# Performance work log

Hardware: AMD Instinct MI355X
Metric: run time of the kernel (lower is better)

Reference implementation:

```python
import jax, jax.numpy as jnp
import numpy as np

N_NODES = 100000

def gcn_conv(x, W, b, src, dst, norm, n):
    # PyG GCNConv: h = x @ W, then normalized sum-aggregation at target nodes, + bias
    h = x @ W                                   # [N, out]
    msg = h[src] * norm[:, None]                # gather + scale, [E, out]
    out = jax.ops.segment_sum(msg, dst, num_segments=n)
    return out + b

def build_norm(src, dst, n):
    # symmetric normalization with unit edge weights (gcn_norm)
    deg = jax.ops.segment_sum(jnp.ones(src.shape[0], jnp.float32), dst, num_segments=n)
    dinv = jnp.where(deg > 0, jax.lax.rsqrt(jnp.maximum(deg, 1.0)), 0.0)
    return dinv[src] * dinv[dst]

def setup_inputs() -> dict:
    key = jax.random.key(0)
    ks = jax.random.split(key, 10)
    n, e, din, dout = N_NODES, 1600000, 256, 86
    x = jax.random.normal(ks[0], (n, din), jnp.float32)
    edge_index = jax.random.randint(ks[1], (2, e), 0, n, jnp.int64)
    def glorot(k, i, o):
        s = jnp.sqrt(6.0 / (i + o))
        return jax.random.uniform(k, (i, o), jnp.float32, -s, s)
    return {
        'x': x, 'edge_index': edge_index,
        'W1': glorot(ks[2], din, 128), 'b1': jnp.zeros((128,), jnp.float32),
        'W2': glorot(ks[3], 128, 64),  'b2': jnp.zeros((64,), jnp.float32),
        'W3': glorot(ks[4], 64, 32),   'b3': jnp.zeros((32,), jnp.float32),
        'Wc': glorot(ks[5], 32, dout), 'bc': jnp.zeros((dout,), jnp.float32),
    }

def reference(x, edge_index, W1, b1, W2, b2, W3, b3, Wc, bc):
    n = x.shape[0]
    # add self-loops (GCNConv default add_self_loops=True)
    loops = jnp.arange(n, dtype=edge_index.dtype)
    src = jnp.concatenate([edge_index[0], loops])
    dst = jnp.concatenate([edge_index[1], loops])
    norm = build_norm(src, dst, n)
    h = jnp.tanh(gcn_conv(x, W1, b1, src, dst, norm, n))
    h = jnp.tanh(gcn_conv(h, W2, b2, src, dst, norm, n))
    h = jnp.tanh(gcn_conv(h, W3, b3, src, dst, norm, n))
    out = h @ Wc + bc
    return (out, h)
```

## Files before the change

### kernel.cpp

```cpp
#include <hip/hip_runtime.h>
#include <hip/hip_bf16.h>


__global__ void count_kernel(const int* __restrict__ dst, int* __restrict__ count, int E) {
    int e = blockIdx.x * blockDim.x + threadIdx.x;
    if (e < E) atomicAdd(&count[dst[e]], 1);
}

__global__ void scan1_kernel(const int* __restrict__ count, int* __restrict__ incl,
                             float* __restrict__ dinv, int* __restrict__ blocksum, int n) {
    __shared__ int lds[1024];
    int t = threadIdx.x;
    int i = blockIdx.x * 1024 + t;
    int v = (i < n) ? count[i] : 0;
    if (i < n) dinv[i] = rsqrtf((float)(v + 1));
    lds[t] = v;
    __syncthreads();
    for (int off = 1; off < 1024; off <<= 1) {
        int add = (t >= off) ? lds[t - off] : 0;
        __syncthreads();
        lds[t] += add;
        __syncthreads();
    }
    if (i < n) incl[i] = lds[t];
    if (t == 1023) blocksum[blockIdx.x] = lds[1023];
}

__global__ void scan2_kernel(const int* __restrict__ blocksum, int* __restrict__ blockoff,
                             int* __restrict__ rowptr, int nb, int n, int E) {
    __shared__ int lds[1024];
    int t = threadIdx.x;
    int v = (t < nb) ? blocksum[t] : 0;
    lds[t] = v;
    __syncthreads();
    for (int off = 1; off < 1024; off <<= 1) {
        int add = (t >= off) ? lds[t - off] : 0;
        __syncthreads();
        lds[t] += add;
        __syncthreads();
    }
    if (t < nb) blockoff[t] = lds[t] - v;
    if (t == 0) rowptr[n] = E;
}

__global__ void scan3_kernel(int* __restrict__ rowptr, const int* __restrict__ count,
                             const int* __restrict__ blockoff, int n) {
    int i = blockIdx.x * blockDim.x + threadIdx.x;
    if (i < n) rowptr[i] = rowptr[i] - count[i] + blockoff[i >> 10];
}

__global__ void scatter_kernel(const int* __restrict__ src, const int* __restrict__ dst,
                               const int* __restrict__ rowptr, int* __restrict__ cursor,
                               int* __restrict__ esrc, int E) {
    int e = blockIdx.x * blockDim.x + threadIdx.x;
    if (e < E) {
        int d = dst[e];
        int pos = rowptr[d] + atomicAdd(&cursor[d], 1);
        esrc[pos] = src[e];
    }
}

template<int DIN, int DOUT, int TN>
__global__ __launch_bounds__(256) void matmul_scale_kernel(
        const float* __restrict__ X, const float* __restrict__ W,
        const float* __restrict__ dinv, float* __restrict__ G, int n) {
    constexpr int TM = 8;
    constexpr int NCG = DOUT / TN;
    constexpr int NRG = 256 / NCG;
    constexpr int BM = NRG * TM;
    constexpr int BK = 32;
    constexpr int XS = BM + 4;

    __shared__ float Xt[BK][XS];
    __shared__ float Ws[BK][DOUT];

    int tid = threadIdx.x;
    int tx = tid % NCG;
    int ty = tid / NCG;
    int row0 = blockIdx.x * BM;

    float acc[TM][TN];
    #pragma unroll
    for (int r = 0; r < TM; r++)
        #pragma unroll
        for (int c = 0; c < TN; c++) acc[r][c] = 0.f;

    for (int k0 = 0; k0 < DIN; k0 += BK) {
        #pragma unroll
        for (int i = tid; i < BM * (BK / 4); i += 256) {
            int r  = i >> 3;
            int c4 = (i & 7) << 2;
            int rg = row0 + r;
            float4 v = make_float4(0.f, 0.f, 0.f, 0.f);
            if (rg < n) v = *(const float4*)&X[(size_t)rg * DIN + k0 + c4];
            const float* vp = (const float*)&v;
            #pragma unroll
            for (int j = 0; j < 4; j++) {
                int c  = c4 + j;
                int rs = r ^ (((c >> 2) & 3) << 3);
                Xt[c][rs] = vp[j];
            }
        }
        #pragma unroll
        for (int i = tid; i < BK * (DOUT / 4); i += 256) {
            int r  = i / (DOUT / 4);
            int c4 = (i % (DOUT / 4)) << 2;
            *(float4*)&Ws[r][c4] = *(const float4*)&W[(size_t)(k0 + r) * DOUT + c4];
        }
        __syncthreads();

        #pragma unroll 4
        for (int k = 0; k < BK; k++) {
            int mask = ((k >> 2) & 3) << 3;
            int rr = (ty * TM) ^ mask;
            float xv[TM];
            *(float4*)&xv[0] = *(const float4*)&Xt[k][rr];
            *(float4*)&xv[4] = *(const float4*)&Xt[k][rr + 4];
            float wv[TN];
            #pragma unroll
            for (int c4 = 0; c4 < TN; c4 += 4)
                *(float4*)&wv[c4] = *(const float4*)&Ws[k][tx * TN + c4];
            #pragma unroll
            for (int r = 0; r < TM; r++)
                #pragma unroll
                for (int c = 0; c < TN; c++)
                    acc[r][c] += xv[r] * wv[c];
        }
        __syncthreads();
    }

    #pragma unroll
    for (int r = 0; r < TM; r++) {
        int rg = row0 + ty * TM + r;
        if (rg < n) {
            float di = dinv[rg];
            float ov[TN];
            #pragma unroll
            for (int c = 0; c < TN; c++) ov[c] = acc[r][c] * di;
            #pragma unroll
            for (int c4 = 0; c4 < TN; c4 += 4)
                *(float4*)&G[(size_t)rg * DOUT + tx * TN + c4] = *(float4*)&ov[c4];
        }
    }
}

template<int DOUT>
__global__ void agg_kernel(const float* __restrict__ g, const float* __restrict__ dinv,
                           const int* __restrict__ rowptr, const int* __restrict__ esrc,
                           const float* __restrict__ bias, float* __restrict__ out, int n) {
    constexpr int LPN = DOUT / 2;
    constexpr int NPW = 64 / LPN;
    int wave = threadIdx.x >> 6;
    int lane = threadIdx.x & 63;
    int sub  = lane / LPN;
    int cl   = lane % LPN;
    int node = (blockIdx.x * (blockDim.x >> 6) + wave) * NPW + sub;
    if (node >= n) return;

    const float2* g2 = (const float2*)g;
    float2 acc = g2[(size_t)node * LPN + cl];

    int e = rowptr[node], end = rowptr[node + 1];
    for (; e + 4 <= end; e += 4) {
        int s0 = esrc[e], s1 = esrc[e + 1], s2 = esrc[e + 2], s3 = esrc[e + 3];
        float2 v0 = g2[(size_t)s0 * LPN + cl];
        float2 v1 = g2[(size_t)s1 * LPN + cl];
        float2 v2 = g2[(size_t)s2 * LPN + cl];
        float2 v3 = g2[(size_t)s3 * LPN + cl];
        acc.x += v0.x + v1.x + v2.x + v3.x;
        acc.y += v0.y + v1.y + v2.y + v3.y;
    }
    for (; e < end; e++) {
        int s = esrc[e];
        float2 v = g2[(size_t)s * LPN + cl];
        acc.x += v.x;
        acc.y += v.y;
    }
    float di = dinv[node];
    float2 b = ((const float2*)bias)[cl];
    float2 o;
    o.x = tanhf(di * acc.x + b.x);
    o.y = tanhf(di * acc.y + b.y);
    ((float2*)out)[(size_t)node * LPN + cl] = o;
}

__global__ __launch_bounds__(256) void cls_kernel(
        const float* __restrict__ H, const float* __restrict__ Wc,
        const float* __restrict__ bc, float* __restrict__ out, int n) {
    constexpr int DIN = 32, DOUT = 86, RPB = 64;
    __shared__ float Hs[RPB][DIN + 4];
    __shared__ float Ws[DIN][DOUT];
    __shared__ float bs[DOUT];
    int tid = threadIdx.x;
    int row0 = blockIdx.x * RPB;
    for (int i = tid; i < DIN * DOUT; i += 256) Ws[i / DOUT][i % DOUT] = Wc[i];
    if (tid < DOUT) bs[tid] = bc[tid];
    for (int i = tid; i < RPB * (DIN / 4); i += 256) {
        int r = i >> 3, c4 = (i & 7) << 2;
        int rg = row0 + r;
        float4 v = make_float4(0.f, 0.f, 0.f, 0.f);
        if (rg < n) v = *(const float4*)&H[(size_t)rg * DIN + c4];
        *(float4*)&Hs[r][c4] = v;
    }
    __syncthreads();
    for (int idx = tid; idx < RPB * DOUT; idx += 256) {
        int r = idx / DOUT, c = idx - r * DOUT;
        float a = bs[c];
        #pragma unroll
        for (int k = 0; k < DIN; k++) a += Hs[r][k] * Ws[k][c];
        int rg = row0 + r;
        if (rg < n) out[(size_t)rg * DOUT + c] = a;
    }
}

extern "C" void kernel_launch(void* const* d_in, const int* in_sizes, int n_in,
                              void* d_out, int out_size, void* d_ws, size_t ws_size,
                              hipStream_t stream) {
    const float* x  = (const float*)d_in[0];
    const int*   ei = (const int*)d_in[1];
    const float* W1 = (const float*)d_in[2];
    const float* b1 = (const float*)d_in[3];
    const float* W2 = (const float*)d_in[4];
    const float* b2 = (const float*)d_in[5];
    const float* W3 = (const float*)d_in[6];
    const float* b3 = (const float*)d_in[7];
    const float* Wc = (const float*)d_in[8];
    const float* bc = (const float*)d_in[9];

    const int n = in_sizes[0] / 256;
    const int E = in_sizes[1] / 2;
    const int* src = ei;
    const int* dst = ei + E;

    char* ws = (char*)d_ws;
    size_t off = 0;
    auto alloc = [&](size_t bytes) {
        void* p = ws + off;
        off = (off + bytes + 255) & ~(size_t)255;
        return p;
    };
    float* dinv    = (float*)alloc((size_t)n * 4);
    int*   count   = (int*)  alloc((size_t)n * 4);
    int*   rowptr  = (int*)  alloc((size_t)(n + 1) * 4);
    int*   cursor  = (int*)  alloc((size_t)n * 4);
    int*   blocksum= (int*)  alloc(1024 * 4);
    int*   blockoff= (int*)  alloc(1024 * 4);
    int*   esrc    = (int*)  alloc((size_t)E * 4);
    float* bufA    = (float*)alloc((size_t)n * 128 * 4);
    float* bufB    = (float*)alloc((size_t)n * 128 * 4);

    float* outp = (float*)d_out;
    float* h3   = outp + (size_t)n * 86;

    hipMemsetAsync(count, 0, (size_t)n * 4, stream);
    hipMemsetAsync(cursor, 0, (size_t)n * 4, stream);

    int eblocks = (E + 255) / 256;
    count_kernel<<<eblocks, 256, 0, stream>>>(dst, count, E);
    int nb = (n + 1023) / 1024;
    scan1_kernel<<<nb, 1024, 0, stream>>>(count, rowptr, dinv, blocksum, n);
    scan2_kernel<<<1, 1024, 0, stream>>>(blocksum, blockoff, rowptr, nb, n, E);
    scan3_kernel<<<(n + 255) / 256, 256, 0, stream>>>(rowptr, count, blockoff, n);
    scatter_kernel<<<eblocks, 256, 0, stream>>>(src, dst, rowptr, cursor, esrc, E);

    matmul_scale_kernel<256, 128, 8><<<(n + 127) / 128, 256, 0, stream>>>(x, W1, dinv, bufA, n);
    agg_kernel<128><<<(n + 3) / 4, 256, 0, stream>>>(bufA, dinv, rowptr, esrc, b1, bufB, n);
    matmul_scale_kernel<128, 64, 4><<<(n + 127) / 128, 256, 0, stream>>>(bufB, W2, dinv, bufA, n);
    agg_kernel<64><<<(n + 7) / 8, 256, 0, stream>>>(bufA, dinv, rowptr, esrc, b2, bufB, n);
    matmul_scale_kernel<64, 32, 4><<<(n + 255) / 256, 256, 0, stream>>>(bufB, W3, dinv, bufA, n);
    agg_kernel<32><<<(n + 15) / 16, 256, 0, stream>>>(bufA, dinv, rowptr, esrc, b3, h3, n);
    cls_kernel<<<(n + 63) / 64, 256, 0, stream>>>(h3, Wc, bc, outp, n);
}
```

Before: 709.7 us.

## Store scaled GEMM outputs in fp16 to halve aggregation gather traffic

The per-layer transformed features are written as packed half precision instead of fp32. The aggregation kernels then gather 8-byte fp16 quads per lane and accumulate in fp32. The matmul kernel is retiled to 128-thread blocks with smaller row tiles and interleaved column groups, and the launch geometry changes to match. The aim is to cut the random-gather memory traffic in aggregation, which dominates, at the cost of fp16 rounding error in the intermediate features.

```diff
diff --git a/kernel.cpp b/kernel.cpp
--- a/kernel.cpp
+++ b/kernel.cpp
@@ -1,5 +1,6 @@
 #include <hip/hip_runtime.h>
 #include <hip/hip_bf16.h>
+#include <hip/hip_fp16.h>
 
 
 __global__ void count_kernel(const int* __restrict__ dst, int* __restrict__ count, int E) {
@@ -60,14 +61,14 @@
     }
 }
 
-template<int DIN, int DOUT, int TN>
-__global__ __launch_bounds__(256) void matmul_scale_kernel(
+template<int DIN, int DOUT, int QN, int BM>
+__global__ __launch_bounds__(128) void matmul_scale_kernel(
         const float* __restrict__ X, const float* __restrict__ W,
-        const float* __restrict__ dinv, float* __restrict__ G, int n) {
+        const float* __restrict__ dinv, __half* __restrict__ G, int n) {
     constexpr int TM = 8;
-    constexpr int NCG = DOUT / TN;
-    constexpr int NRG = 256 / NCG;
-    constexpr int BM = NRG * TM;
+    constexpr int NCG = DOUT / (4 * QN);
+    constexpr int NRG = BM / TM;
+    static_assert(NCG * NRG == 128, "block must be 128 threads");
     constexpr int BK = 32;
     constexpr int XS = BM + 4;
 
@@ -79,30 +80,28 @@
     int ty = tid / NCG;
     int row0 = blockIdx.x * BM;
 
-    float acc[TM][TN];
+    float acc[TM][4 * QN];
     #pragma unroll
     for (int r = 0; r < TM; r++)
         #pragma unroll
-        for (int c = 0; c < TN; c++) acc[r][c] = 0.f;
+        for (int c = 0; c < 4 * QN; c++) acc[r][c] = 0.f;
 
     for (int k0 = 0; k0 < DIN; k0 += BK) {
         #pragma unroll
-        for (int i = tid; i < BM * (BK / 4); i += 256) {
+        for (int i = tid; i < BM * (BK / 4); i += 128) {
             int r  = i >> 3;
             int c4 = (i & 7) << 2;
             int rg = row0 + r;
             float4 v = make_float4(0.f, 0.f, 0.f, 0.f);
             if (rg < n) v = *(const float4*)&X[(size_t)rg * DIN + k0 + c4];
-            const float* vp = (const float*)&v;
-            #pragma unroll
-            for (int j = 0; j < 4; j++) {
-                int c  = c4 + j;
-                int rs = r ^ (((c >> 2) & 3) << 3);
-                Xt[c][rs] = vp[j];
-            }
-        }
-        #pragma unroll
-        for (int i = tid; i < BK * (DOUT / 4); i += 256) {
+            int rs = r ^ ((i & 3) << 3);
+            Xt[c4 + 0][rs] = v.x;
+            Xt[c4 + 1][rs] = v.y;
+            Xt[c4 + 2][rs] = v.z;
+            Xt[c4 + 3][rs] = v.w;
+        }
+        #pragma unroll
+        for (int i = tid; i < BK * (DOUT / 4); i += 128) {
             int r  = i / (DOUT / 4);
             int c4 = (i % (DOUT / 4)) << 2;
             *(float4*)&Ws[r][c4] = *(const float4*)&W[(size_t)(k0 + r) * DOUT + c4];
@@ -111,19 +110,18 @@
 
         #pragma unroll 4
         for (int k = 0; k < BK; k++) {
-            int mask = ((k >> 2) & 3) << 3;
-            int rr = (ty * TM) ^ mask;
+            int rr = (ty * TM) ^ (((k >> 2) & 3) << 3);
             float xv[TM];
             *(float4*)&xv[0] = *(const float4*)&Xt[k][rr];
             *(float4*)&xv[4] = *(const float4*)&Xt[k][rr + 4];
-            float wv[TN];
+            float wv[4 * QN];
             #pragma unroll
-            for (int c4 = 0; c4 < TN; c4 += 4)
-                *(float4*)&wv[c4] = *(const float4*)&Ws[k][tx * TN + c4];
+            for (int q = 0; q < QN; q++)
+                *(float4*)&wv[q * 4] = *(const float4*)&Ws[k][(tx + q * NCG) * 4];
             #pragma unroll
             for (int r = 0; r < TM; r++)
                 #pragma unroll
-                for (int c = 0; c < TN; c++)
+                for (int c = 0; c < 4 * QN; c++)
                     acc[r][c] += xv[r] * wv[c];
         }
         __syncthreads();
@@ -134,21 +132,24 @@
         int rg = row0 + ty * TM + r;
         if (rg < n) {
             float di = dinv[rg];
-            float ov[TN];
             #pragma unroll
-            for (int c = 0; c < TN; c++) ov[c] = acc[r][c] * di;
-            #pragma unroll
-            for (int c4 = 0; c4 < TN; c4 += 4)
-                *(float4*)&G[(size_t)rg * DOUT + tx * TN + c4] = *(float4*)&ov[c4];
+            for (int q = 0; q < QN; q++) {
+                __half2 p0 = __floats2half2_rn(acc[r][q * 4 + 0] * di, acc[r][q * 4 + 1] * di);
+                __half2 p1 = __floats2half2_rn(acc[r][q * 4 + 2] * di, acc[r][q * 4 + 3] * di);
+                uint2 w;
+                w.x = *reinterpret_cast<unsigned int*>(&p0);
+                w.y = *reinterpret_cast<unsigned int*>(&p1);
+                *(uint2*)&G[(size_t)rg * DOUT + (tx + q * NCG) * 4] = w;
+            }
         }
     }
 }
 
 template<int DOUT>
-__global__ void agg_kernel(const float* __restrict__ g, const float* __restrict__ dinv,
+__global__ void agg_kernel(const __half* __restrict__ g, const float* __restrict__ dinv,
                            const int* __restrict__ rowptr, const int* __restrict__ esrc,
                            const float* __restrict__ bias, float* __restrict__ out, int n) {
-    constexpr int LPN = DOUT / 2;
+    constexpr int LPN = DOUT / 4;
     constexpr int NPW = 64 / LPN;
     int wave = threadIdx.x >> 6;
     int lane = threadIdx.x & 63;
@@ -157,31 +158,34 @@
     int node = (blockIdx.x * (blockDim.x >> 6) + wave) * NPW + sub;
     if (node >= n) return;
 
-    const float2* g2 = (const float2*)g;
-    float2 acc = g2[(size_t)node * LPN + cl];
+    const uint2* g2 = (const uint2*)g;
+    auto fetch = [&](int s, float4& a) {
+        uint2 v = g2[(size_t)s * LPN + cl];
+        __half2 h0 = *reinterpret_cast<__half2*>(&v.x);
+        __half2 h1 = *reinterpret_cast<__half2*>(&v.y);
+        float2 f0 = __half22float2(h0);
+        float2 f1 = __half22float2(h1);
+        a.x += f0.x; a.y += f0.y; a.z += f1.x; a.w += f1.y;
+    };
+
+    float4 acc = make_float4(0.f, 0.f, 0.f, 0.f);
+    fetch(node, acc);
 
     int e = rowptr[node], end = rowptr[node + 1];
     for (; e + 4 <= end; e += 4) {
         int s0 = esrc[e], s1 = esrc[e + 1], s2 = esrc[e + 2], s3 = esrc[e + 3];
-        float2 v0 = g2[(size_t)s0 * LPN + cl];
-        float2 v1 = g2[(size_t)s1 * LPN + cl];
-        float2 v2 = g2[(size_t)s2 * LPN + cl];
-        float2 v3 = g2[(size_t)s3 * LPN + cl];
-        acc.x += v0.x + v1.x + v2.x + v3.x;
-        acc.y += v0.y + v1.y + v2.y + v3.y;
-    }
-    for (; e < end; e++) {
-        int s = esrc[e];
-        float2 v = g2[(size_t)s * LPN + cl];
-        acc.x += v.x;
-        acc.y += v.y;
-    }
+        fetch(s0, acc); fetch(s1, acc); fetch(s2, acc); fetch(s3, acc);
+    }
+    for (; e < end; e++) fetch(esrc[e], acc);
+
     float di = dinv[node];
-    float2 b = ((const float2*)bias)[cl];
-    float2 o;
+    float4 b = *(const float4*)&bias[cl * 4];
+    float4 o;
     o.x = tanhf(di * acc.x + b.x);
     o.y = tanhf(di * acc.y + b.y);
-    ((float2*)out)[(size_t)node * LPN + cl] = o;
+    o.z = tanhf(di * acc.z + b.z);
+    o.w = tanhf(di * acc.w + b.w);
+    *(float4*)&out[(size_t)node * DOUT + cl * 4] = o;
 }
 
 __global__ __launch_bounds__(256) void cls_kernel(
@@ -239,15 +243,15 @@
         off = (off + bytes + 255) & ~(size_t)255;
         return p;
     };
-    float* dinv    = (float*)alloc((size_t)n * 4);
-    int*   count   = (int*)  alloc((size_t)n * 4);
-    int*   rowptr  = (int*)  alloc((size_t)(n + 1) * 4);
-    int*   cursor  = (int*)  alloc((size_t)n * 4);
-    int*   blocksum= (int*)  alloc(1024 * 4);
-    int*   blockoff= (int*)  alloc(1024 * 4);
-    int*   esrc    = (int*)  alloc((size_t)E * 4);
-    float* bufA    = (float*)alloc((size_t)n * 128 * 4);
-    float* bufB    = (float*)alloc((size_t)n * 128 * 4);
+    float*  dinv    = (float*)alloc((size_t)n * 4);
+    int*    count   = (int*)  alloc((size_t)n * 4);
+    int*    rowptr  = (int*)  alloc((size_t)(n + 1) * 4);
+    int*    cursor  = (int*)  alloc((size_t)n * 4);
+    int*    blocksum= (int*)  alloc(1024 * 4);
+    int*    blockoff= (int*)  alloc(1024 * 4);
+    int*    esrc    = (int*)  alloc((size_t)E * 4);
+    __half* Gh      = (__half*)alloc((size_t)n * 128 * 2);
+    float*  Hf      = (float*)alloc((size_t)n * 128 * 4);
 
     float* outp = (float*)d_out;
     float* h3   = outp + (size_t)n * 86;
@@ -263,11 +267,11 @@
     scan3_kernel<<<(n + 255) / 256, 256, 0, stream>>>(rowptr, count, blockoff, n);
     scatter_kernel<<<eblocks, 256, 0, stream>>>(src, dst, rowptr, cursor, esrc, E);
 
-    matmul_scale_kernel<256, 128, 8><<<(n + 127) / 128, 256, 0, stream>>>(x, W1, dinv, bufA, n);
-    agg_kernel<128><<<(n + 3) / 4, 256, 0, stream>>>(bufA, dinv, rowptr, esrc, b1, bufB, n);
-    matmul_scale_kernel<128, 64, 4><<<(n + 127) / 128, 256, 0, stream>>>(bufB, W2, dinv, bufA, n);
-    agg_kernel<64><<<(n + 7) / 8, 256, 0, stream>>>(bufA, dinv, rowptr, esrc, b2, bufB, n);
-    matmul_scale_kernel<64, 32, 4><<<(n + 255) / 256, 256, 0, stream>>>(bufB, W3, dinv, bufA, n);
-    agg_kernel<32><<<(n + 15) / 16, 256, 0, stream>>>(bufA, dinv, rowptr, esrc, b3, h3, n);
+    matmul_scale_kernel<256, 128, 2, 64><<<(n + 63) / 64, 128, 0, stream>>>(x, W1, dinv, Gh, n);
+    agg_kernel<128><<<(n + 7) / 8, 256, 0, stream>>>(Gh, dinv, rowptr, esrc, b1, Hf, n);
+    matmul_scale_kernel<128, 64, 1, 64><<<(n + 63) / 64, 128, 0, stream>>>(Hf, W2, dinv, Gh, n);
+    agg_kernel<64><<<(n + 15) / 16, 256, 0, stream>>>(Gh, dinv, rowptr, esrc, b2, Hf, n);
+    matmul_scale_kernel<64, 32, 1, 128><<<(n + 127) / 128, 128, 0, stream>>>(Hf, W3, dinv, Gh, n);
+    agg_kernel<32><<<(n + 31) / 32, 256, 0, stream>>>(Gh, dinv, rowptr, esrc, b3, h3, n);
     cls_kernel<<<(n + 63) / 64, 256, 0, stream>>>(h3, Wc, bc, outp, n);
 }
```

Measured after the change: 682.7 us. 3.8% less time.
